# Performance work log

Measured on AMD Instinct MI355X. Metric: run time of the kernel, lower is better.

The kernel has to match this reference:

```python
import jax, jax.numpy as jnp
import numpy as np

N, E, IN, HID, H, OUT, G = 20000, 320000, 128, 64, 6, 10, 64
NEG_SLOPE = 0.2


def gat_conv(x, W, a_src, a_dst, b, src, dst):
    # x: [N, F_in]; W: [F_in, H*C]; a_src/a_dst: [H, C]; b: [H*C]
    n = x.shape[0]
    h = (x @ W).reshape(n, H, HID)                      # [N, H, C]
    alpha_s = jnp.einsum('nhc,hc->nh', h, a_src)        # [N, H]
    alpha_d = jnp.einsum('nhc,hc->nh', h, a_dst)
    e = jax.nn.leaky_relu(alpha_s[src] + alpha_d[dst], NEG_SLOPE)  # [E, H]
    # segment softmax over incoming edges of each destination node
    m = jax.ops.segment_max(e, dst, num_segments=n)
    ex = jnp.exp(e - m[dst])
    s = jax.ops.segment_sum(ex, dst, num_segments=n)
    alpha = ex / (s[dst] + 1e-16)                       # [E, H]
    out = jax.ops.segment_sum(alpha[:, :, None] * h[src], dst, num_segments=n)
    return out.reshape(n, H * HID) + b


def setup_inputs() -> dict:
    key = jax.random.key(0)
    ks = jax.random.split(key, 24)
    p = lambda k, shp: jax.random.normal(k, shp, dtype=jnp.float32) * 0.1
    inp = {
        'x': jax.random.normal(ks[0], (N, IN), dtype=jnp.float32),
        'edge_index': jax.random.randint(ks[1], (2, E), 0, N),
        'batch': jnp.sort(jax.random.randint(ks[2], (N,), 0, G)),
        'W1': p(ks[3], (IN, H * HID)), 'a1_src': p(ks[4], (H, HID)), 'a1_dst': p(ks[5], (H, HID)), 'b1': p(ks[6], (H * HID,)),
        'W2': p(ks[7], (H * HID, H * HID)), 'a2_src': p(ks[8], (H, HID)), 'a2_dst': p(ks[9], (H, HID)), 'b2': p(ks[10], (H * HID,)),
        'Ws1': p(ks[11], (IN, H * HID)), 'as1_src': p(ks[12], (H, HID)), 'as1_dst': p(ks[13], (H, HID)), 'bs1': p(ks[14], (H * HID,)),
        'Ws2': p(ks[15], (H * HID, H * HID)), 'as2_src': p(ks[16], (H, HID)), 'as2_dst': p(ks[17], (H, HID)), 'bs2': p(ks[18], (H * HID,)),
        'r1_w': p(ks[19], (H * HID, HID)), 'r1_b': p(ks[20], (HID,)),
        'r2_w': p(ks[21], (HID, OUT)), 'r2_b': p(ks[22], (OUT,)),
    }
    return inp


def reference(x, edge_index, batch, W1, a1_src, a1_dst, b1, W2, a2_src, a2_dst, b2,
              Ws1, as1_src, as1_dst, bs1, Ws2, as2_src, as2_dst, bs2,
              r1_w, r1_b, r2_w, r2_b):
    # PyG GATConv adds self-loops by default
    loop = jnp.arange(N, dtype=edge_index.dtype)
    src = jnp.concatenate([edge_index[0], loop])
    dst = jnp.concatenate([edge_index[1], loop])

    # skip branch (dropout = identity in eval)
    xs = jax.nn.relu(gat_conv(x, Ws1, as1_src, as1_dst, bs1, src, dst))
    xs = jax.nn.relu(gat_conv(xs, Ws2, as2_src, as2_dst, bs2, src, dst))

    # main branch
    h = jax.nn.relu(gat_conv(x, W1, a1_src, a1_dst, b1, src, dst))
    h = jax.nn.relu(gat_conv(h, W2, a2_src, a2_dst, b2, src, dst))

    h = h + xs

    # global mean pool over graphs
    sums = jax.ops.segment_sum(h, batch, num_segments=G)          # [G, H*C]
    cnts = jax.ops.segment_sum(jnp.ones((N,), h.dtype), batch, num_segments=G)
    x_readout = sums / jnp.maximum(cnts, 1.0)[:, None]

    x_global = jax.nn.relu(x_readout @ r1_w + r1_b) @ r2_w + r2_b  # [G, OUT]
    return (jnp.squeeze(x_global), x_readout)
```

## Files before the change

kernel.cpp:

```cpp
#include <hip/hip_runtime.h>
#include <hip/hip_fp16.h>

#define NN 20000
#define EE 320000
#define ETOT 340000
#define FIN 128
#define NH 6
#define FF 384
#define NOUT 10
#define NG 64
#define NEG 0.2f
#define PCH 32
#define NB ((NN + 255) / 256)
#define NBLK ((NN + 3) / 4)

typedef short short8 __attribute__((ext_vector_type(8)));
typedef float f32x4 __attribute__((ext_vector_type(4)));

__device__ __half g_h16[2][(size_t)NN * FF];
__device__ unsigned short g_feat[2][(size_t)NN * FF];
__device__ unsigned short g_xHi[(size_t)NN * FIN];
__device__ unsigned short g_WtHi[4][FF * FF];
__device__ float g_alS[4][NN * NH];
__device__ float g_alD[4][NN * NH];
__device__ int g_rowptr[NN + 1];
__device__ int g_cnt[NN];
__device__ int g_cur[NN];
__device__ int g_blocksum[NB];
__device__ int g_colsrc[ETOT];
__device__ float g_pool[NG * FF];
__device__ int g_gcnt[NG];

__device__ __forceinline__ unsigned short f2bf(float f) {
  unsigned u = __float_as_uint(f);
  u += 0x7FFFu + ((u >> 16) & 1u);
  return (unsigned short)(u >> 16);
}
__device__ __forceinline__ float bf2f(unsigned short s) {
  return __uint_as_float(((unsigned)s) << 16);
}

__device__ __forceinline__ void gl_lds16(const void* g, void* l) {
  __builtin_amdgcn_global_load_lds(
      (const __attribute__((address_space(1))) unsigned int*)(unsigned long long)g,
      (__attribute__((address_space(3))) unsigned int*)(unsigned int)(unsigned long long)l,
      16, 0, 0);
}

__device__ __forceinline__ void mfma_acc(f32x4& c, short8 a, short8 b) {
  asm("v_mfma_f32_16x16x32_bf16 %0, %1, %2, %0" : "+v"(c) : "v"(a), "v"(b));
}

__device__ __forceinline__ void fmix(float2& acc, unsigned hv, float w) {
  asm("v_fma_mix_f32 %0, %2, %3, %0 op_sel:[0,0,0] op_sel_hi:[1,0,0]\n\t"
      "v_fma_mix_f32 %1, %2, %3, %1 op_sel:[1,0,0] op_sel_hi:[1,0,0]"
      : "+v"(acc.x), "+v"(acc.y)
      : "v"(hv), "v"(w));
}

__global__ __launch_bounds__(256) void k_prep(const float* __restrict__ xin,
                                              const float* __restrict__ Ws1,
                                              const float* __restrict__ Ws2,
                                              const float* __restrict__ W1,
                                              const float* __restrict__ W2) {
  const int tid = blockIdx.x * 256 + threadIdx.x;
  const int stride = gridDim.x * 256;
  for (int i = tid; i < FIN * FF; i += stride) {
    int k = i / FF, c = i % FF;
    g_WtHi[0][c * FIN + k] = f2bf(Ws1[i]);
    g_WtHi[2][c * FIN + k] = f2bf(W1[i]);
  }
  for (int i = tid; i < FF * FF; i += stride) {
    int k = i / FF, c = i % FF;
    g_WtHi[1][c * FF + k] = f2bf(Ws2[i]);
    g_WtHi[3][c * FF + k] = f2bf(W2[i]);
  }
  for (int i = tid; i < NN; i += stride) g_cnt[i] = 0;
  for (int i = tid; i < NG * FF; i += stride) g_pool[i] = 0.f;
  for (int i = tid; i < NG; i += stride) g_gcnt[i] = 0;
  for (int i = tid; i < 4 * NN * NH; i += stride) {
    (&g_alS[0][0])[i] = 0.f;
    (&g_alD[0][0])[i] = 0.f;
  }
  const float4* s4 = (const float4*)xin;
  ushort4* oh4 = (ushort4*)g_xHi;
  for (int i = tid; i < (NN * FIN) >> 2; i += stride) {
    float4 v = s4[i];
    ushort4 h;
    h.x = f2bf(v.x); h.y = f2bf(v.y); h.z = f2bf(v.z); h.w = f2bf(v.w);
    oh4[i] = h;
  }
}

__global__ __launch_bounds__(256) void k_hist(const int* __restrict__ ei) {
  int i = blockIdx.x * 256 + threadIdx.x;
  if (i >= ETOT) return;
  int d = (i < EE) ? ei[EE + i] : (i - EE);
  atomicAdd(&g_cnt[d], 1);
}

__global__ __launch_bounds__(256) void k_scan_blk() {
  int b = blockIdx.x;
  int tid = threadIdx.x;
  int i = b * 256 + tid;
  int lane = tid & 63, wid = tid >> 6;
  int v = (i < NN) ? g_cnt[i] : 0;
  int s = v;
  #pragma unroll
  for (int off = 1; off < 64; off <<= 1) {
    int t = __shfl_up(s, off);
    if (lane >= off) s += t;
  }
  __shared__ int wsum[4];
  if (lane == 63) wsum[wid] = s;
  __syncthreads();
  int woff = 0;
  #pragma unroll
  for (int w = 0; w < 4; ++w) woff += (w < wid) ? wsum[w] : 0;
  if (i < NN) g_rowptr[i] = woff + s - v;
  if (tid == 0) g_blocksum[b] = wsum[0] + wsum[1] + wsum[2] + wsum[3];
}

__global__ __launch_bounds__(128) void k_scan_top() {
  int tid = threadIdx.x;
  int lane = tid & 63, wid = tid >> 6;
  int v = (tid < NB) ? g_blocksum[tid] : 0;
  int s = v;
  #pragma unroll
  for (int off = 1; off < 64; off <<= 1) {
    int t = __shfl_up(s, off);
    if (lane >= off) s += t;
  }
  __shared__ int wsum[2];
  if (lane == 63) wsum[wid] = s;
  __syncthreads();
  int woff = (wid == 1) ? wsum[0] : 0;
  int excl = woff + s - v;
  if (tid < NB) g_blocksum[tid] = excl;
  if (tid == NB - 1) g_rowptr[NN] = excl + v;
}

__global__ __launch_bounds__(256) void k_scan_add() {
  int i = blockIdx.x * 256 + threadIdx.x;
  if (i >= NN) return;
  int r = g_rowptr[i] + g_blocksum[blockIdx.x];
  g_rowptr[i] = r;
  g_cur[i] = r;
}

__global__ __launch_bounds__(256) void k_scatter(const int* __restrict__ ei) {
  int i = blockIdx.x * 256 + threadIdx.x;
  if (i >= ETOT) return;
  int s, d;
  if (i < EE) { s = ei[i]; d = ei[EE + i]; } else { s = d = i - EE; }
  int pos = atomicAdd(&g_cur[d], 1);
  g_colsrc[pos] = s;
}

__global__ __launch_bounds__(256) void k_gemm(int lvl,
                                              const float* __restrict__ asr0,
                                              const float* __restrict__ adt0,
                                              const float* __restrict__ asr1,
                                              const float* __restrict__ adt1) {
  __shared__ unsigned short lA[128 * 64];
  __shared__ unsigned short lB[128 * 64];
  const int br = blockIdx.z;
  const int layer = (lvl ? 1 : 0) + (br ? 2 : 0);
  const int widx = layer;
  const int K = lvl ? FF : FIN;
  const unsigned short* Ah = lvl ? g_feat[br] : g_xHi;
  const unsigned short* Bh = g_WtHi[widx];
  const float* asr = br ? asr1 : asr0;
  const float* adt = br ? adt1 : adt0;
  __half* hout = g_h16[br];
  const int m0 = blockIdx.x * 128;
  const int n0 = blockIdx.y * 128;
  const int tid = threadIdx.x;
  const int wave = tid >> 6, lane = tid & 63;
  const int wm = wave >> 1, wn = wave & 1;
  const int srow = lane >> 3;
  const int scol = (lane & 7) * 8;

  f32x4 acc[4][4] = {};

  for (int k0 = 0; k0 < K; k0 += 64) {
    __syncthreads();
    #pragma unroll
    for (int it = 0; it < 4; ++it) {
      int c = wave * 4 + it;
      int rA = c * 8 + srow;
      int gr = m0 + rA; gr = (gr < NN) ? gr : (NN - 1);
      gl_lds16(Ah + (size_t)gr * K + k0 + scol, (unsigned short*)lA + c * 512);
      int cB = n0 + rA;
      gl_lds16(Bh + (size_t)cB * K + k0 + scol, (unsigned short*)lB + c * 512);
    }
    __syncthreads();
    #pragma unroll
    for (int kk = 0; kk < 64; kk += 32) {
      const int kb = kk + (lane >> 4) * 8;
      const int r16 = lane & 15;
      short8 af[4], bfr[4];
      #pragma unroll
      for (int mf = 0; mf < 4; ++mf)
        af[mf] = *(const short8*)&lA[(wm * 64 + mf * 16 + r16) * 64 + kb];
      #pragma unroll
      for (int nf = 0; nf < 4; ++nf)
        bfr[nf] = *(const short8*)&lB[(wn * 64 + nf * 16 + r16) * 64 + kb];
      #pragma unroll
      for (int mf = 0; mf < 4; ++mf)
        #pragma unroll
        for (int nf = 0; nf < 4; ++nf)
          mfma_acc(acc[mf][nf], af[mf], bfr[nf]);
    }
  }
  asm volatile("s_nop 7\n\ts_nop 7" :::);

  const int r16 = lane & 15;
  #pragma unroll
  for (int mf = 0; mf < 4; ++mf) {
    #pragma unroll
    for (int nf = 0; nf < 4; ++nf) {
      int col = n0 + wn * 64 + nf * 16 + r16;
      int rb = m0 + wm * 64 + mf * 16 + ((lane >> 4) << 2);
      #pragma unroll
      for (int j = 0; j < 4; ++j) {
        int r = rb + j;
        if (r < NN) hout[(size_t)r * FF + col] = __float2half(acc[mf][nf][j]);
      }
    }
  }
  const int hd = blockIdx.y * 2 + wn;
  float as_v[4], ad_v[4];
  #pragma unroll
  for (int nf = 0; nf < 4; ++nf) {
    as_v[nf] = asr[hd * 64 + nf * 16 + r16];
    ad_v[nf] = adt[hd * 64 + nf * 16 + r16];
  }
  float* alS = g_alS[layer];
  float* alD = g_alD[layer];
  #pragma unroll
  for (int mf = 0; mf < 4; ++mf) {
    #pragma unroll
    for (int j = 0; j < 4; ++j) {
      float ps = 0.f, pd = 0.f;
      #pragma unroll
      for (int nf = 0; nf < 4; ++nf) {
        ps = fmaf(acc[mf][nf][j], as_v[nf], ps);
        pd = fmaf(acc[mf][nf][j], ad_v[nf], pd);
      }
      #pragma unroll
      for (int off = 1; off < 16; off <<= 1) {
        ps += __shfl_xor(ps, off);
        pd += __shfl_xor(pd, off);
      }
      int r = m0 + wm * 64 + mf * 16 + ((lane >> 4) << 2) + j;
      if (r16 == 0 && r < NN) {
        atomicAdd(&alS[r * NH + hd], ps);
        atomicAdd(&alD[r * NH + hd], pd);
      }
    }
  }
}

__global__ __launch_bounds__(256) void k_edge(int lvl,
                                              const float* __restrict__ bias0,
                                              const float* __restrict__ bias1) {
  __shared__ int l_se[4][64];
  __shared__ float l_wf[4][NH][64];
  int wv = threadIdx.x >> 6;
  int node = blockIdx.x * 4 + wv;
  int lane = threadIdx.x & 63;
  if (node >= NN) return;
  const int br = blockIdx.y;
  const int layer = (lvl ? 1 : 0) + (br ? 2 : 0);
  const float* bias = br ? bias1 : bias0;
  const __half* htab = g_h16[br];
  const float* aS = g_alS[layer];
  const float* aD = g_alD[layer];
  const int lo = g_rowptr[node], hi = g_rowptr[node + 1];
  const int deg = hi - lo;
  float ad[NH];
  #pragma unroll
  for (int h = 0; h < NH; ++h) ad[h] = aD[node * NH + h];

  const bool hiHalf = (lane >= 32);
  float m[NH], inv[NH];
  const bool fast = (deg <= 64);

  if (fast) {
    bool val = lane < deg;
    int s = val ? g_colsrc[lo + lane] : 0;
    const float2* ap = (const float2*)(aS + (size_t)s * NH);
    float2 p0 = ap[0], p1 = ap[1], p2 = ap[2];
    float v[NH] = {p0.x + ad[0], p0.y + ad[1], p1.x + ad[2],
                   p1.y + ad[3], p2.x + ad[4], p2.y + ad[5]};
    float mm[NH], w[NH], ss[NH];
    #pragma unroll
    for (int h = 0; h < NH; ++h) {
      v[h] = (v[h] > 0.f) ? v[h] : NEG * v[h];
      mm[h] = val ? v[h] : -1e30f;
    }
    #pragma unroll
    for (int h = 0; h < NH; ++h)
      #pragma unroll
      for (int off = 32; off > 0; off >>= 1)
        mm[h] = fmaxf(mm[h], __shfl_xor(mm[h], off));
    #pragma unroll
    for (int h = 0; h < NH; ++h) {
      w[h] = val ? __expf(v[h] - mm[h]) : 0.f;
      ss[h] = w[h];
    }
    #pragma unroll
    for (int h = 0; h < NH; ++h)
      #pragma unroll
      for (int off = 32; off > 0; off >>= 1)
        ss[h] += __shfl_xor(ss[h], off);
    l_se[wv][lane] = s;
    #pragma unroll
    for (int h = 0; h < NH; ++h)
      l_wf[wv][h][lane] = w[h] * __frcp_rn(ss[h] + 1e-16f);
  } else {
    #pragma unroll
    for (int h = 0; h < NH; ++h) m[h] = -1e30f;
    for (int e = lo + lane; e < hi; e += 64) {
      int se = g_colsrc[e];
      #pragma unroll
      for (int h = 0; h < NH; ++h) {
        float v = aS[se * NH + h] + ad[h];
        v = (v > 0.f) ? v : NEG * v;
        m[h] = fmaxf(m[h], v);
      }
    }
    #pragma unroll
    for (int h = 0; h < NH; ++h)
      #pragma unroll
      for (int off = 32; off > 0; off >>= 1)
        m[h] = fmaxf(m[h], __shfl_xor(m[h], off));
    float ss[NH] = {0.f, 0.f, 0.f, 0.f, 0.f, 0.f};
    for (int e = lo + lane; e < hi; e += 64) {
      int se = g_colsrc[e];
      #pragma unroll
      for (int h = 0; h < NH; ++h) {
        float v = aS[se * NH + h] + ad[h];
        v = (v > 0.f) ? v : NEG * v;
        ss[h] += __expf(v - m[h]);
      }
    }
    #pragma unroll
    for (int h = 0; h < NH; ++h) {
      #pragma unroll
      for (int off = 32; off > 0; off >>= 1)
        ss[h] += __shfl_xor(ss[h], off);
      inv[h] = __frcp_rn(ss[h] + 1e-16f);
    }
  }

  float2 accA[3] = {{0.f,0.f},{0.f,0.f},{0.f,0.f}};
  float2 accB[3] = {{0.f,0.f},{0.f,0.f},{0.f,0.f}};
  float2 accC[3] = {{0.f,0.f},{0.f,0.f},{0.f,0.f}};
  float2 accD[3] = {{0.f,0.f},{0.f,0.f},{0.f,0.f}};

  if (fast) {
    const int h0 = hiHalf ? 1 : 0, h1 = hiHalf ? 3 : 2, h2 = hiHalf ? 5 : 4;
    const int degR = (deg + 3) & ~3;
    for (int e = 0; e < degR; e += 4) {
      int4 se4 = *(int4*)&l_se[wv][e];
      float4 w0 = *(float4*)&l_wf[wv][h0][e];
      float4 w1 = *(float4*)&l_wf[wv][h1][e];
      float4 w2 = *(float4*)&l_wf[wv][h2][e];
      const unsigned* r0 = (const unsigned*)(htab + (size_t)se4.x * FF) + lane;
      const unsigned* r1 = (const unsigned*)(htab + (size_t)se4.y * FF) + lane;
      const unsigned* r2 = (const unsigned*)(htab + (size_t)se4.z * FF) + lane;
      const unsigned* r3 = (const unsigned*)(htab + (size_t)se4.w * FF) + lane;
      unsigned ha[3] = {r0[0], r0[64], r0[128]};
      unsigned hb[3] = {r1[0], r1[64], r1[128]};
      unsigned hc[3] = {r2[0], r2[64], r2[128]};
      unsigned hd[3] = {r3[0], r3[64], r3[128]};
      fmix(accA[0], ha[0], w0.x); fmix(accB[0], hb[0], w0.y);
      fmix(accC[0], hc[0], w0.z); fmix(accD[0], hd[0], w0.w);
      fmix(accA[1], ha[1], w1.x); fmix(accB[1], hb[1], w1.y);
      fmix(accC[1], hc[1], w1.z); fmix(accD[1], hd[1], w1.w);
      fmix(accA[2], ha[2], w2.x); fmix(accB[2], hb[2], w2.y);
      fmix(accC[2], hc[2], w2.z); fmix(accD[2], hd[2], w2.w);
    }
  } else {
    for (int e = 0; e < deg; ++e) {
      int se = g_colsrc[lo + e];
      const float* as = aS + (size_t)se * NH;
      float we[NH];
      #pragma unroll
      for (int h = 0; h < NH; ++h) {
        float v = as[h] + ad[h];
        v = (v > 0.f) ? v : NEG * v;
        we[h] = __expf(v - m[h]) * inv[h];
      }
      float wa[3] = {hiHalf ? we[1] : we[0], hiHalf ? we[3] : we[2],
                     hiHalf ? we[5] : we[4]};
      const unsigned* r0 = (const unsigned*)(htab + (size_t)se * FF) + lane;
      unsigned h0v[3] = {r0[0], r0[64], r0[128]};
      #pragma unroll
      for (int c = 0; c < 3; ++c) fmix(accA[c], h0v[c], wa[c]);
    }
  }

  #pragma unroll
  for (int c = 0; c < 3; ++c) {
    float2 bv = *(const float2*)(bias + c * 128 + lane * 2);
    float ox = fmaxf(accA[c].x + accB[c].x + accC[c].x + accD[c].x + bv.x, 0.f);
    float oy = fmaxf(accA[c].y + accB[c].y + accC[c].y + accD[c].y + bv.y, 0.f);
    size_t off = (size_t)node * FF + c * 128 + lane * 2;
    ushort2 hh2 = {f2bf(ox), f2bf(oy)};
    *(ushort2*)(g_feat[br] + off) = hh2;
  }
}

__global__ __launch_bounds__(384) void k_pool_acc(const int* __restrict__ batch) {
  int n0 = blockIdx.x * PCH;
  if (n0 >= NN) return;
  int n1 = n0 + PCH; if (n1 > NN) n1 = NN;
  int d = threadIdx.x;
  int cur = batch[n0];
  float acc = 0.f;
  int cnt = 0;
  for (int n = n0; n < n1; ++n) {
    int g = batch[n];
    if (g != cur) {
      atomicAdd(&g_pool[cur * FF + d], acc);
      if (d == 0) atomicAdd(&g_gcnt[cur], cnt);
      acc = 0.f; cnt = 0; cur = g;
    }
    acc += bf2f(g_feat[0][(size_t)n * FF + d]) + bf2f(g_feat[1][(size_t)n * FF + d]);
    ++cnt;
  }
  atomicAdd(&g_pool[cur * FF + d], acc);
  if (d == 0) atomicAdd(&g_gcnt[cur], cnt);
}

__global__ __launch_bounds__(384) void k_finish(const float* __restrict__ r1w,
                                                const float* __restrict__ r1b,
                                                const float* __restrict__ r2w,
                                                const float* __restrict__ r2b,
                                                float* __restrict__ dout) {
  int g = blockIdx.x;
  int d = threadIdx.x;
  __shared__ float xr[FF];
  __shared__ float hid[64];
  int cnt = g_gcnt[g];
  float denom = (cnt > 0) ? (float)cnt : 1.f;
  float v = g_pool[g * FF + d] / denom;
  xr[d] = v;
  dout[NG * NOUT + g * FF + d] = v;
  __syncthreads();
  if (d < 64) {
    float acc = r1b[d];
    for (int k = 0; k < FF; ++k) acc = fmaf(xr[k], r1w[k * 64 + d], acc);
    hid[d] = fmaxf(acc, 0.f);
  }
  __syncthreads();
  if (d < NOUT) {
    float o = r2b[d];
    #pragma unroll
    for (int j = 0; j < 64; ++j) o = fmaf(hid[j], r2w[j * NOUT + d], o);
    dout[g * NOUT + d] = o;
  }
}

extern "C" void kernel_launch(void* const* d_in, const int* in_sizes, int n_in,
                              void* d_out, int out_size, void* d_ws, size_t ws_size,
                              hipStream_t stream) {
  const float* x    = (const float*)d_in[0];
  const int* ei     = (const int*)d_in[1];
  const int* batch  = (const int*)d_in[2];
  const float* W1   = (const float*)d_in[3];
  const float* a1s  = (const float*)d_in[4];
  const float* a1d  = (const float*)d_in[5];
  const float* b1   = (const float*)d_in[6];
  const float* W2   = (const float*)d_in[7];
  const float* a2s  = (const float*)d_in[8];
  const float* a2d  = (const float*)d_in[9];
  const float* b2   = (const float*)d_in[10];
  const float* Ws1  = (const float*)d_in[11];
  const float* as1s = (const float*)d_in[12];
  const float* as1d = (const float*)d_in[13];
  const float* bs1  = (const float*)d_in[14];
  const float* Ws2  = (const float*)d_in[15];
  const float* as2s = (const float*)d_in[16];
  const float* as2d = (const float*)d_in[17];
  const float* bs2  = (const float*)d_in[18];
  const float* r1w  = (const float*)d_in[19];
  const float* r1b  = (const float*)d_in[20];
  const float* r2w  = (const float*)d_in[21];
  const float* r2b  = (const float*)d_in[22];
  float* out = (float*)d_out;

  dim3 b256(256);
  k_prep<<<dim3(2048), b256, 0, stream>>>(x, Ws1, Ws2, W1, W2);
  k_hist<<<dim3((ETOT + 255) / 256), b256, 0, stream>>>(ei);
  k_scan_blk<<<dim3(NB), b256, 0, stream>>>();
  k_scan_top<<<dim3(1), dim3(128), 0, stream>>>();
  k_scan_add<<<dim3(NB), b256, 0, stream>>>();
  k_scatter<<<dim3((ETOT + 255) / 256), b256, 0, stream>>>(ei);

  dim3 gemmGrid((NN + 127) / 128, FF / 128, 2);
  dim3 edgeGrid(NBLK, 2);

  k_gemm<<<gemmGrid, b256, 0, stream>>>(0, as1s, as1d, a1s, a1d);
  k_edge<<<edgeGrid, b256, 0, stream>>>(0, bs1, b1);
  k_gemm<<<gemmGrid, b256, 0, stream>>>(1, as2s, as2d, a2s, a2d);
  k_edge<<<edgeGrid, b256, 0, stream>>>(1, bs2, b2);
  k_pool_acc<<<dim3((NN + PCH - 1) / PCH), dim3(384), 0, stream>>>(batch);
  k_finish<<<dim3(NG), dim3(384), 0, stream>>>(r1w, r1b, r2w, r2b, out);
}
```

Measured before the change: 311.3 us.

## Merge both GAT branches into a single edge-aggregation pass per node

Result: slower. 342.9 us (+10.1%).

```diff
diff --git a/kernel.cpp b/kernel.cpp
--- a/kernel.cpp
+++ b/kernel.cpp
@@ -13,6 +13,7 @@
 #define PCH 32
 #define NB ((NN + 255) / 256)
 #define NBLK ((NN + 3) / 4)
+#define TBLOFF (NN * 192)
 
 typedef short short8 __attribute__((ext_vector_type(8)));
 typedef float f32x4 __attribute__((ext_vector_type(4)));
@@ -266,151 +267,178 @@
                                               const float* __restrict__ bias0,
                                               const float* __restrict__ bias1) {
   __shared__ int l_se[4][64];
-  __shared__ float l_wf[4][NH][64];
+  __shared__ float l_wf[4][2][NH][64];
   int wv = threadIdx.x >> 6;
   int node = blockIdx.x * 4 + wv;
   int lane = threadIdx.x & 63;
   if (node >= NN) return;
-  const int br = blockIdx.y;
-  const int layer = (lvl ? 1 : 0) + (br ? 2 : 0);
-  const float* bias = br ? bias1 : bias0;
-  const __half* htab = g_h16[br];
-  const float* aS = g_alS[layer];
-  const float* aD = g_alD[layer];
   const int lo = g_rowptr[node], hi = g_rowptr[node + 1];
   const int deg = hi - lo;
-  float ad[NH];
-  #pragma unroll
-  for (int h = 0; h < NH; ++h) ad[h] = aD[node * NH + h];
-
   const bool hiHalf = (lane >= 32);
-  float m[NH], inv[NH];
   const bool fast = (deg <= 64);
+  float m[2][NH], inv[2][NH];
 
   if (fast) {
     bool val = lane < deg;
     int s = val ? g_colsrc[lo + lane] : 0;
-    const float2* ap = (const float2*)(aS + (size_t)s * NH);
-    float2 p0 = ap[0], p1 = ap[1], p2 = ap[2];
-    float v[NH] = {p0.x + ad[0], p0.y + ad[1], p1.x + ad[2],
-                   p1.y + ad[3], p2.x + ad[4], p2.y + ad[5]};
-    float mm[NH], w[NH], ss[NH];
-    #pragma unroll
-    for (int h = 0; h < NH; ++h) {
-      v[h] = (v[h] > 0.f) ? v[h] : NEG * v[h];
-      mm[h] = val ? v[h] : -1e30f;
-    }
-    #pragma unroll
-    for (int h = 0; h < NH; ++h)
-      #pragma unroll
-      for (int off = 32; off > 0; off >>= 1)
-        mm[h] = fmaxf(mm[h], __shfl_xor(mm[h], off));
-    #pragma unroll
-    for (int h = 0; h < NH; ++h) {
-      w[h] = val ? __expf(v[h] - mm[h]) : 0.f;
-      ss[h] = w[h];
-    }
-    #pragma unroll
-    for (int h = 0; h < NH; ++h)
-      #pragma unroll
-      for (int off = 32; off > 0; off >>= 1)
-        ss[h] += __shfl_xor(ss[h], off);
     l_se[wv][lane] = s;
     #pragma unroll
-    for (int h = 0; h < NH; ++h)
-      l_wf[wv][h][lane] = w[h] * __frcp_rn(ss[h] + 1e-16f);
+    for (int b = 0; b < 2; ++b) {
+      const int layer = (lvl ? 1 : 0) + (b ? 2 : 0);
+      const float* aS = g_alS[layer];
+      const float* aD = g_alD[layer] + (size_t)node * NH;
+      const float2* ap = (const float2*)(aS + (size_t)s * NH);
+      float2 p0 = ap[0], p1 = ap[1], p2 = ap[2];
+      float v[NH] = {p0.x + aD[0], p0.y + aD[1], p1.x + aD[2],
+                     p1.y + aD[3], p2.x + aD[4], p2.y + aD[5]};
+      float mm[NH], w[NH], ss[NH];
+      #pragma unroll
+      for (int h = 0; h < NH; ++h) {
+        v[h] = (v[h] > 0.f) ? v[h] : NEG * v[h];
+        mm[h] = val ? v[h] : -1e30f;
+      }
+      #pragma unroll
+      for (int h = 0; h < NH; ++h)
+        #pragma unroll
+        for (int off = 32; off > 0; off >>= 1)
+          mm[h] = fmaxf(mm[h], __shfl_xor(mm[h], off));
+      #pragma unroll
+      for (int h = 0; h < NH; ++h) {
+        w[h] = val ? __expf(v[h] - mm[h]) : 0.f;
+        ss[h] = w[h];
+      }
+      #pragma unroll
+      for (int h = 0; h < NH; ++h)
+        #pragma unroll
+        for (int off = 32; off > 0; off >>= 1)
+          ss[h] += __shfl_xor(ss[h], off);
+      #pragma unroll
+      for (int h = 0; h < NH; ++h)
+        l_wf[wv][b][h][lane] = w[h] * __frcp_rn(ss[h] + 1e-16f);
+    }
   } else {
     #pragma unroll
-    for (int h = 0; h < NH; ++h) m[h] = -1e30f;
-    for (int e = lo + lane; e < hi; e += 64) {
-      int se = g_colsrc[e];
+    for (int b = 0; b < 2; ++b) {
+      const int layer = (lvl ? 1 : 0) + (b ? 2 : 0);
+      const float* aS = g_alS[layer];
+      const float* aD = g_alD[layer] + (size_t)node * NH;
+      float ad[NH];
+      #pragma unroll
+      for (int h = 0; h < NH; ++h) ad[h] = aD[h];
+      #pragma unroll
+      for (int h = 0; h < NH; ++h) m[b][h] = -1e30f;
+      for (int e = lo + lane; e < hi; e += 64) {
+        int se = g_colsrc[e];
+        #pragma unroll
+        for (int h = 0; h < NH; ++h) {
+          float v = aS[se * NH + h] + ad[h];
+          v = (v > 0.f) ? v : NEG * v;
+          m[b][h] = fmaxf(m[b][h], v);
+        }
+      }
+      #pragma unroll
+      for (int h = 0; h < NH; ++h)
+        #pragma unroll
+        for (int off = 32; off > 0; off >>= 1)
+          m[b][h] = fmaxf(m[b][h], __shfl_xor(m[b][h], off));
+      float ss[NH] = {0.f, 0.f, 0.f, 0.f, 0.f, 0.f};
+      for (int e = lo + lane; e < hi; e += 64) {
+        int se = g_colsrc[e];
+        #pragma unroll
+        for (int h = 0; h < NH; ++h) {
+          float v = aS[se * NH + h] + ad[h];
+          v = (v > 0.f) ? v : NEG * v;
+          ss[h] += __expf(v - m[b][h]);
+        }
+      }
       #pragma unroll
       for (int h = 0; h < NH; ++h) {
-        float v = aS[se * NH + h] + ad[h];
-        v = (v > 0.f) ? v : NEG * v;
-        m[h] = fmaxf(m[h], v);
-      }
-    }
-    #pragma unroll
-    for (int h = 0; h < NH; ++h)
-      #pragma unroll
-      for (int off = 32; off > 0; off >>= 1)
-        m[h] = fmaxf(m[h], __shfl_xor(m[h], off));
-    float ss[NH] = {0.f, 0.f, 0.f, 0.f, 0.f, 0.f};
-    for (int e = lo + lane; e < hi; e += 64) {
-      int se = g_colsrc[e];
-      #pragma unroll
-      for (int h = 0; h < NH; ++h) {
-        float v = aS[se * NH + h] + ad[h];
-        v = (v > 0.f) ? v : NEG * v;
-        ss[h] += __expf(v - m[h]);
-      }
-    }
-    #pragma unroll
-    for (int h = 0; h < NH; ++h) {
-      #pragma unroll
-      for (int off = 32; off > 0; off >>= 1)
-        ss[h] += __shfl_xor(ss[h], off);
-      inv[h] = __frcp_rn(ss[h] + 1e-16f);
-    }
-  }
-
-  float2 accA[3] = {{0.f,0.f},{0.f,0.f},{0.f,0.f}};
-  float2 accB[3] = {{0.f,0.f},{0.f,0.f},{0.f,0.f}};
-  float2 accC[3] = {{0.f,0.f},{0.f,0.f},{0.f,0.f}};
-  float2 accD[3] = {{0.f,0.f},{0.f,0.f},{0.f,0.f}};
+        #pragma unroll
+        for (int off = 32; off > 0; off >>= 1)
+          ss[h] += __shfl_xor(ss[h], off);
+        inv[b][h] = __frcp_rn(ss[h] + 1e-16f);
+      }
+    }
+  }
+
+  float2 aA[2][3] = {};
+  float2 aB[2][3] = {};
 
   if (fast) {
     const int h0 = hiHalf ? 1 : 0, h1 = hiHalf ? 3 : 2, h2 = hiHalf ? 5 : 4;
     const int degR = (deg + 3) & ~3;
     for (int e = 0; e < degR; e += 4) {
       int4 se4 = *(int4*)&l_se[wv][e];
-      float4 w0 = *(float4*)&l_wf[wv][h0][e];
-      float4 w1 = *(float4*)&l_wf[wv][h1][e];
-      float4 w2 = *(float4*)&l_wf[wv][h2][e];
-      const unsigned* r0 = (const unsigned*)(htab + (size_t)se4.x * FF) + lane;
-      const unsigned* r1 = (const unsigned*)(htab + (size_t)se4.y * FF) + lane;
-      const unsigned* r2 = (const unsigned*)(htab + (size_t)se4.z * FF) + lane;
-      const unsigned* r3 = (const unsigned*)(htab + (size_t)se4.w * FF) + lane;
-      unsigned ha[3] = {r0[0], r0[64], r0[128]};
-      unsigned hb[3] = {r1[0], r1[64], r1[128]};
-      unsigned hc[3] = {r2[0], r2[64], r2[128]};
-      unsigned hd[3] = {r3[0], r3[64], r3[128]};
-      fmix(accA[0], ha[0], w0.x); fmix(accB[0], hb[0], w0.y);
-      fmix(accC[0], hc[0], w0.z); fmix(accD[0], hd[0], w0.w);
-      fmix(accA[1], ha[1], w1.x); fmix(accB[1], hb[1], w1.y);
-      fmix(accC[1], hc[1], w1.z); fmix(accD[1], hd[1], w1.w);
-      fmix(accA[2], ha[2], w2.x); fmix(accB[2], hb[2], w2.y);
-      fmix(accC[2], hc[2], w2.z); fmix(accD[2], hd[2], w2.w);
+      float4 w00 = *(float4*)&l_wf[wv][0][h0][e];
+      float4 w01 = *(float4*)&l_wf[wv][0][h1][e];
+      float4 w02 = *(float4*)&l_wf[wv][0][h2][e];
+      float4 w10 = *(float4*)&l_wf[wv][1][h0][e];
+      float4 w11 = *(float4*)&l_wf[wv][1][h1][e];
+      float4 w12 = *(float4*)&l_wf[wv][1][h2][e];
+      const unsigned* r0 = (const unsigned*)(g_h16[0] + (size_t)se4.x * FF) + lane;
+      const unsigned* r1 = (const unsigned*)(g_h16[0] + (size_t)se4.y * FF) + lane;
+      const unsigned* r2 = (const unsigned*)(g_h16[0] + (size_t)se4.z * FF) + lane;
+      const unsigned* r3 = (const unsigned*)(g_h16[0] + (size_t)se4.w * FF) + lane;
+      unsigned a0[3] = {r0[0], r0[64], r0[128]};
+      unsigned a1[3] = {r1[0], r1[64], r1[128]};
+      unsigned a2[3] = {r2[0], r2[64], r2[128]};
+      unsigned a3[3] = {r3[0], r3[64], r3[128]};
+      unsigned b0[3] = {r0[TBLOFF], r0[TBLOFF + 64], r0[TBLOFF + 128]};
+      unsigned b1[3] = {r1[TBLOFF], r1[TBLOFF + 64], r1[TBLOFF + 128]};
+      unsigned b2[3] = {r2[TBLOFF], r2[TBLOFF + 64], r2[TBLOFF + 128]};
+      unsigned b3[3] = {r3[TBLOFF], r3[TBLOFF + 64], r3[TBLOFF + 128]};
+      fmix(aA[0][0], a0[0], w00.x); fmix(aB[0][0], a1[0], w00.y);
+      fmix(aA[0][0], a2[0], w00.z); fmix(aB[0][0], a3[0], w00.w);
+      fmix(aA[0][1], a0[1], w01.x); fmix(aB[0][1], a1[1], w01.y);
+      fmix(aA[0][1], a2[1], w01.z); fmix(aB[0][1], a3[1], w01.w);
+      fmix(aA[0][2], a0[2], w02.x); fmix(aB[0][2], a1[2], w02.y);
+      fmix(aA[0][2], a2[2], w02.z); fmix(aB[0][2], a3[2], w02.w);
+      fmix(aA[1][0], b0[0], w10.x); fmix(aB[1][0], b1[0], w10.y);
+      fmix(aA[1][0], b2[0], w10.z); fmix(aB[1][0], b3[0], w10.w);
+      fmix(aA[1][1], b0[1], w11.x); fmix(aB[1][1], b1[1], w11.y);
+      fmix(aA[1][1], b2[1], w11.z); fmix(aB[1][1], b3[1], w11.w);
+      fmix(aA[1][2], b0[2], w12.x); fmix(aB[1][2], b1[2], w12.y);
+      fmix(aA[1][2], b2[2], w12.z); fmix(aB[1][2], b3[2], w12.w);
     }
   } else {
     for (int e = 0; e < deg; ++e) {
       int se = g_colsrc[lo + e];
-      const float* as = aS + (size_t)se * NH;
-      float we[NH];
-      #pragma unroll
-      for (int h = 0; h < NH; ++h) {
-        float v = as[h] + ad[h];
-        v = (v > 0.f) ? v : NEG * v;
-        we[h] = __expf(v - m[h]) * inv[h];
-      }
-      float wa[3] = {hiHalf ? we[1] : we[0], hiHalf ? we[3] : we[2],
-                     hiHalf ? we[5] : we[4]};
-      const unsigned* r0 = (const unsigned*)(htab + (size_t)se * FF) + lane;
-      unsigned h0v[3] = {r0[0], r0[64], r0[128]};
-      #pragma unroll
-      for (int c = 0; c < 3; ++c) fmix(accA[c], h0v[c], wa[c]);
-    }
-  }
-
-  #pragma unroll
-  for (int c = 0; c < 3; ++c) {
-    float2 bv = *(const float2*)(bias + c * 128 + lane * 2);
-    float ox = fmaxf(accA[c].x + accB[c].x + accC[c].x + accD[c].x + bv.x, 0.f);
-    float oy = fmaxf(accA[c].y + accB[c].y + accC[c].y + accD[c].y + bv.y, 0.f);
-    size_t off = (size_t)node * FF + c * 128 + lane * 2;
-    ushort2 hh2 = {f2bf(ox), f2bf(oy)};
-    *(ushort2*)(g_feat[br] + off) = hh2;
+      const unsigned* r0 = (const unsigned*)(g_h16[0] + (size_t)se * FF) + lane;
+      unsigned av[3] = {r0[0], r0[64], r0[128]};
+      unsigned bv[3] = {r0[TBLOFF], r0[TBLOFF + 64], r0[TBLOFF + 128]};
+      #pragma unroll
+      for (int b = 0; b < 2; ++b) {
+        const int layer = (lvl ? 1 : 0) + (b ? 2 : 0);
+        const float* as = g_alS[layer] + (size_t)se * NH;
+        const float* aD = g_alD[layer] + (size_t)node * NH;
+        float we[NH];
+        #pragma unroll
+        for (int h = 0; h < NH; ++h) {
+          float v = as[h] + aD[h];
+          v = (v > 0.f) ? v : NEG * v;
+          we[h] = __expf(v - m[b][h]) * inv[b][h];
+        }
+        float wa[3] = {hiHalf ? we[1] : we[0], hiHalf ? we[3] : we[2],
+                       hiHalf ? we[5] : we[4]};
+        const unsigned* rv = b ? bv : av;
+        #pragma unroll
+        for (int c = 0; c < 3; ++c) fmix(aA[b][c], rv[c], wa[c]);
+      }
+    }
+  }
+
+  #pragma unroll
+  for (int b = 0; b < 2; ++b) {
+    const float* bias = b ? bias1 : bias0;
+    #pragma unroll
+    for (int c = 0; c < 3; ++c) {
+      float2 bv = *(const float2*)(bias + c * 128 + lane * 2);
+      float ox = fmaxf(aA[b][c].x + aB[b][c].x + bv.x, 0.f);
+      float oy = fmaxf(aA[b][c].y + aB[b][c].y + bv.y, 0.f);
+      size_t off = (size_t)node * FF + c * 128 + lane * 2;
+      ushort2 hh2 = {f2bf(ox), f2bf(oy)};
+      *(ushort2*)(g_feat[b] + off) = hh2;
+    }
   }
 }
 
@@ -502,7 +530,7 @@
   k_scatter<<<dim3((ETOT + 255) / 256), b256, 0, stream>>>(ei);
 
   dim3 gemmGrid((NN + 127) / 128, FF / 128, 2);
-  dim3 edgeGrid(NBLK, 2);
+  dim3 edgeGrid(NBLK);
 
   k_gemm<<<gemmGrid, b256, 0, stream>>>(0, as1s, as1d, a1s, a1d);
   k_edge<<<edgeGrid, b256, 0, stream>>>(0, bs1, b1);
```
